# Kernel optimization log

Hardware: AMD Instinct MI355X
Metric: run time of the kernel (lower is better)

Reference implementation:

```python
import jax, jax.numpy as jnp
import numpy as np

B, L, D, H = 2, 2048, 1024, 16
HD = D // H

def setup_inputs() -> dict:
    key = jax.random.key(0)
    ks = jax.random.split(key, 9)
    s = 1.0 / np.sqrt(D)
    return {
        "x": jax.random.normal(ks[0], (B, L, D), jnp.float32),
        "Wq": jax.random.normal(ks[1], (D, D), jnp.float32) * s,
        "bq": jax.random.normal(ks[2], (D,), jnp.float32) * 0.02,
        "Wk": jax.random.normal(ks[3], (D, D), jnp.float32) * s,
        "bk": jax.random.normal(ks[4], (D,), jnp.float32) * 0.02,
        "Wv": jax.random.normal(ks[5], (D, D), jnp.float32) * s,
        "bv": jax.random.normal(ks[6], (D,), jnp.float32) * 0.02,
        "Wo": jax.random.normal(ks[7], (D, D), jnp.float32) * s,
        "bo": jax.random.normal(ks[8], (D,), jnp.float32) * 0.02,
    }

def reference(x, Wq, bq, Wk, bk, Wv, bv, Wo, bo):
    b, l, d = x.shape
    # projections -> [B, H, L, HD]
    def split_heads(t):
        return t.reshape(b, l, H, HD).transpose(0, 2, 1, 3)
    Q = split_heads(x @ Wq + bq)
    K = split_heads(x @ Wk + bk)
    V = split_heads(x @ Wv + bv)
    scores = jnp.einsum('bhqd,bhkd->bhqk', Q, K)  # [B,H,L,L]
    causal = jnp.tril(jnp.ones((l, l), bool))
    scores = jnp.where(causal, scores, -jnp.inf)
    attn = jax.nn.softmax(scores / np.sqrt(HD), axis=-1)
    ctx = jnp.einsum('bhqk,bhkd->bhqd', attn, V)
    ctx = ctx.transpose(0, 2, 1, 3).reshape(b, l, d)
    return ctx @ Wo + bo
```

## Files before the change

### kernel.cpp

```cpp
#include <hip/hip_runtime.h>
#include <stdint.h>

typedef unsigned short u16;
typedef __attribute__((ext_vector_type(8))) __bf16 bf16x8;
typedef __attribute__((ext_vector_type(4))) float f32x4;

#define BM 128
#define BN 128
#define BK 32

__device__ __forceinline__ u16 f2bf(float f) {
  union { float f; uint32_t u; } c; c.f = f;
  uint32_t u = c.u + 0x7fffu + ((c.u >> 16) & 1u);
  return (u16)(u >> 16);
}
__device__ __forceinline__ uint32_t cvtpk(float a, float b) {
  uint32_t r;
  asm("v_cvt_pk_bf16_f32 %0, %1, %2" : "=v"(r) : "v"(a), "v"(b));
  return r;
}

__device__ __forceinline__ void async16(const u16* g, u16* l) {
  __builtin_amdgcn_global_load_lds(
      (const __attribute__((address_space(1))) void*)g,
      (__attribute__((address_space(3))) void*)l, 16, 0, 0);
}

__device__ __forceinline__ f32x4 mfma16(bf16x8 a, bf16x8 b, f32x4 c) {
  return __builtin_amdgcn_mfma_f32_16x16x32_bf16(a, b, c, 0, 0, 0);
}


__global__ __launch_bounds__(256) void x_cvt_kernel(const float* __restrict__ x,
                                                    u16* __restrict__ xb) {
  int i = (blockIdx.x * 256 + threadIdx.x) * 4;
  float4 v = *(const float4*)(x + i);
  uint2 t; t.x = cvtpk(v.x, v.y); t.y = cvtpk(v.z, v.w);
  *(uint2*)(xb + i) = t;
}

__global__ __launch_bounds__(256) void wt_cvt_kernel(const float* __restrict__ Wq,
                                                     const float* __restrict__ Wk,
                                                     const float* __restrict__ Wv,
                                                     const float* __restrict__ Wo,
                                                     u16* __restrict__ out) {
  __shared__ __align__(16) u16 t[64][72];
  int z = blockIdx.z;
  const float* W = (z == 0) ? Wq : (z == 1) ? Wk : (z == 2) ? Wv : Wo;
  u16* o = out + (size_t)z * (1u << 20);
  int n0 = blockIdx.x * 64, k0 = blockIdx.y * 64;
  int tid = threadIdx.x;
  int c4 = (tid & 15) * 4, r0 = tid >> 4;
#pragma unroll
  for (int i = 0; i < 4; i++) {
    int r = r0 + i * 16;
    float4 v = *(const float4*)(W + (size_t)(k0 + r) * 1024 + n0 + c4);
    t[c4 + 0][r] = f2bf(v.x);
    t[c4 + 1][r] = f2bf(v.y);
    t[c4 + 2][r] = f2bf(v.z);
    t[c4 + 3][r] = f2bf(v.w);
  }
  __syncthreads();
  int n = tid >> 2, kc = (tid & 3) * 16;
  uint4 a = *(const uint4*)&t[n][kc];
  uint4 b = *(const uint4*)&t[n][kc + 8];
  *(uint4*)(o + (size_t)(n0 + n) * 1024 + k0 + kc) = a;
  *(uint4*)(o + (size_t)(n0 + n) * 1024 + k0 + kc + 8) = b;
}


__device__ __forceinline__ void gemm_core(const u16* __restrict__ A,
                                          const u16* __restrict__ Bt,
                                          u16* As, u16* Bs, f32x4 (&acc)[4][4]) {
  const int tid = threadIdx.x, wave = tid >> 6, lane = tid & 63;
  const int low = lane & 15, hi = lane >> 4;
  const int wm = wave >> 1, wn = wave & 1;
  const int m0 = blockIdx.y * BM, n0 = blockIdx.x * BN;
  const f32x4 fzero = {0.f, 0.f, 0.f, 0.f};
#pragma unroll
  for (int i = 0; i < 4; i++)
#pragma unroll
    for (int j = 0; j < 4; j++) acc[i][j] = fzero;

  const u16* ap = As + (wm * 64 + low) * BK + hi * 8;
  const u16* bp = Bs + (wn * 64 + low) * BK + hi * 8;

  const int e0 = wave * 128 + lane;
  const int e1 = e0 + 64;
  const u16* ga0 = A + (size_t)(m0 + (e0 >> 2)) * 1024 + (e0 & 3) * 8;
  const u16* ga1 = A + (size_t)(m0 + (e1 >> 2)) * 1024 + (e1 & 3) * 8;
  const u16* gb0 = Bt + (size_t)(n0 + (e0 >> 2)) * 1024 + (e0 & 3) * 8;
  const u16* gb1 = Bt + (size_t)(n0 + (e1 >> 2)) * 1024 + (e1 & 3) * 8;
  u16* la0 = As + (wave * 2 + 0) * 512;
  u16* la1 = As + (wave * 2 + 1) * 512;
  u16* lb0 = Bs + (wave * 2 + 0) * 512;
  u16* lb1 = Bs + (wave * 2 + 1) * 512;

  for (int kt = 0; kt < 1024; kt += BK) {
    __syncthreads();
    async16(ga0 + kt, la0);
    async16(ga1 + kt, la1);
    async16(gb0 + kt, lb0);
    async16(gb1 + kt, lb1);
    __syncthreads();
    bf16x8 af[4], bfv[4];
#pragma unroll
    for (int i = 0; i < 4; i++) af[i] = *(const bf16x8*)(ap + i * 16 * BK);
#pragma unroll
    for (int j = 0; j < 4; j++) bfv[j] = *(const bf16x8*)(bp + j * 16 * BK);
#pragma unroll
    for (int i = 0; i < 4; i++)
#pragma unroll
      for (int j = 0; j < 4; j++) acc[i][j] = mfma16(af[i], bfv[j], acc[i][j]);
  }
}

__global__ __launch_bounds__(256) void gemm_qkv_kernel(
    const u16* __restrict__ xb, const u16* __restrict__ wT,
    const float* __restrict__ bq, const float* __restrict__ bk,
    const float* __restrict__ bv,
    u16* __restrict__ qs, u16* __restrict__ ks, u16* __restrict__ vts) {
  __shared__ __align__(16) u16 As[BM * BK];
  __shared__ __align__(16) u16 Bs[BN * BK];
  const int z = blockIdx.z;
  const u16* Bt = wT + (size_t)z * (1u << 20);
  f32x4 acc[4][4];
  gemm_core(xb, Bt, As, Bs, acc);

  const float* bias = (z == 0) ? bq : (z == 1) ? bk : bv;
  u16* out = (z == 0) ? qs : (z == 1) ? ks : vts;
  const float scale = (z == 0) ? 0.180336880f : 1.0f;
  const int tid = threadIdx.x, wave = tid >> 6, lane = tid & 63;
  const int low = lane & 15, hi = lane >> 4;
  const int wm = wave >> 1, wn = wave & 1;
  const int m0 = blockIdx.y * BM, n0 = blockIdx.x * BN;
#pragma unroll
  for (int i = 0; i < 4; i++)
#pragma unroll
    for (int j = 0; j < 4; j++) {
      int gn = n0 + wn * 64 + j * 16 + low;
      float bval = bias[gn];
      int h = gn >> 6, hd = gn & 63;
#pragma unroll
      for (int r = 0; r < 4; r++) {
        int gm = m0 + wm * 64 + i * 16 + hi * 4 + r;
        int b = gm >> 11, l = gm & 2047;
        float v = (acc[i][j][r] + bval) * scale;
        size_t addr;
        if (z == 2) addr = ((size_t)((b * 16 + h) * 64 + hd)) * 2048 + l;
        else        addr = ((size_t)((b * 16 + h) * 2048 + l)) * 64 + hd;
        out[addr] = f2bf(v);
      }
    }
}

__global__ __launch_bounds__(256) void gemm_out_kernel(
    const u16* __restrict__ ctx, const u16* __restrict__ woT,
    const float* __restrict__ bo, float* __restrict__ out) {
  __shared__ __align__(16) u16 As[BM * BK];
  __shared__ __align__(16) u16 Bs[BN * BK];
  f32x4 acc[4][4];
  gemm_core(ctx, woT, As, Bs, acc);
  const int tid = threadIdx.x, wave = tid >> 6, lane = tid & 63;
  const int low = lane & 15, hi = lane >> 4;
  const int wm = wave >> 1, wn = wave & 1;
  const int m0 = blockIdx.y * BM, n0 = blockIdx.x * BN;
#pragma unroll
  for (int i = 0; i < 4; i++)
#pragma unroll
    for (int j = 0; j < 4; j++) {
      int gn = n0 + wn * 64 + j * 16 + low;
      float bval = bo[gn];
#pragma unroll
      for (int r = 0; r < 4; r++) {
        int gm = m0 + wm * 64 + i * 16 + hi * 4 + r;
        out[(size_t)gm * 1024 + gn] = acc[i][j][r] + bval;
      }
    }
}

#define PSTR 72

__global__ __launch_bounds__(256) void flash_kernel(
    const u16* __restrict__ Qs, const u16* __restrict__ Ks,
    const u16* __restrict__ Vts, u16* __restrict__ ctx) {
  __shared__ __align__(16) u16 Kls[3][64 * 64];
  __shared__ __align__(16) u16 Vls[3][64 * 64];
  __shared__ __align__(16) u16 Pls[8][16 * PSTR];

  const int bid = blockIdx.x;
  const int qt = 15 - (bid >> 5);
  const int bh = bid & 31;
  const int qb = qt * 128;
  const int nkv = 2 * qt + 2;

  const int tid = threadIdx.x, wave = tid >> 6, lane = tid & 63;
  const int low = lane & 15, hi = lane >> 4;
  const int x7 = low & 7;

  const u16* Qb = Qs + (size_t)bh * (2048 * 64);
  const u16* Kb = Ks + (size_t)bh * (2048 * 64);
  const u16* Vb = Vts + (size_t)bh * (64 * 2048);
  const f32x4 fzero = {0.f, 0.f, 0.f, 0.f};

  bf16x8 qf[2][2];
#pragma unroll
  for (int sub = 0; sub < 2; sub++)
#pragma unroll
    for (int dh = 0; dh < 2; dh++)
      qf[sub][dh] = *(const bf16x8*)(Qb + (size_t)(qb + wave * 32 + sub * 16 + low) * 64 + dh * 32 + hi * 8);

  f32x4 o[2][4];
  float m_[2], l_[2];
#pragma unroll
  for (int sub = 0; sub < 2; sub++) {
    m_[sub] = -1e30f; l_[sub] = 0.f;
#pragma unroll
    for (int nt = 0; nt < 4; nt++) o[sub][nt] = fzero;
  }

  const int srow0 = (lane >> 3);
  const int scc = lane & 7;

#define STAGE(buf, KT0)                                                        \
  {                                                                            \
    _Pragma("unroll") for (int i = 0; i < 2; i++) {                            \
      int row = (wave * 2 + i) * 8 + srow0;                                    \
      async16(Kb + (size_t)((KT0) + row) * 64 + ((scc ^ (row & 7)) * 8),       \
              &Kls[buf][(wave * 2 + i) * 512]);                                \
      async16(Vb + (size_t)row * 2048 + (KT0) + ((scc ^ (row & 7)) * 8),       \
              &Vls[buf][(wave * 2 + i) * 512]);                                \
    }                                                                          \
  }

  STAGE(0, 0)
  STAGE(1, 64)

  u16* pls0 = &Pls[wave * 2 + 0][0];
  u16* pls1 = &Pls[wave * 2 + 1][0];
  const int qmax = qb + wave * 32 + 31;

  int c0 = 0, c1 = 1, c2 = 2;
  for (int t = 0; t < nkv; t++) {
    const int kt0 = t * 64;
    if (t + 1 < nkv) { asm volatile("s_waitcnt vmcnt(4)" ::: "memory"); }
    else             { asm volatile("s_waitcnt vmcnt(0)" ::: "memory"); }
    __builtin_amdgcn_s_barrier();
    if (t + 2 < nkv) STAGE(c2, kt0 + 128)

    if (kt0 <= qmax) {
      const u16* Kc = &Kls[c0][0];
      const u16* Vc = &Vls[c0][0];

      f32x4 s[2][4];
      __builtin_amdgcn_s_setprio(1);
#pragma unroll
      for (int nt = 0; nt < 4; nt++) {
        const u16* kb = Kc + (nt * 16 + low) * 64;
        bf16x8 kf0 = *(const bf16x8*)(kb + ((hi ^ x7) * 8));
        bf16x8 kf1 = *(const bf16x8*)(kb + (((4 + hi) ^ x7) * 8));
        s[0][nt] = mfma16(kf0, qf[0][0], fzero);
        s[0][nt] = mfma16(kf1, qf[0][1], s[0][nt]);
        s[1][nt] = mfma16(kf0, qf[1][0], fzero);
        s[1][nt] = mfma16(kf1, qf[1][1], s[1][nt]);
      }
      __builtin_amdgcn_s_setprio(0);

      bf16x8 vf[4][2];
#pragma unroll
      for (int ntd = 0; ntd < 4; ntd++) {
        const u16* vb = Vc + (ntd * 16 + low) * 64;
        vf[ntd][0] = *(const bf16x8*)(vb + ((hi ^ x7) * 8));
        vf[ntd][1] = *(const bf16x8*)(vb + (((4 + hi) ^ x7) * 8));
      }

#pragma unroll
      for (int sub = 0; sub < 2; sub++) {
        const int qsb = qb + wave * 32 + sub * 16;
        if (kt0 + 63 > qsb) {
          const int qrow = qsb + low;
#pragma unroll
          for (int nt = 0; nt < 4; nt++)
#pragma unroll
            for (int r = 0; r < 4; r++) {
              int kg = kt0 + nt * 16 + hi * 4 + r;
              if (kg > qrow) s[sub][nt][r] = -1e30f;
            }
        }
      }

      float pm[2];
#pragma unroll
      for (int sub = 0; sub < 2; sub++) {
        float p = -1e30f;
#pragma unroll
        for (int nt = 0; nt < 4; nt++)
#pragma unroll
          for (int r = 0; r < 4; r++) p = fmaxf(p, s[sub][nt][r]);
        p = fmaxf(p, __shfl_xor(p, 16));
        p = fmaxf(p, __shfl_xor(p, 32));
        pm[sub] = p;
      }
      if (__any((pm[0] > m_[0] + 8.f) || (pm[1] > m_[1] + 8.f))) {
#pragma unroll
        for (int sub = 0; sub < 2; sub++) {
          float mn = fmaxf(m_[sub], pm[sub]);
          float corr = __builtin_amdgcn_exp2f(m_[sub] - mn);
          m_[sub] = mn;
          l_[sub] *= corr;
#pragma unroll
          for (int nt = 0; nt < 4; nt++) {
            o[sub][nt][0] *= corr; o[sub][nt][1] *= corr;
            o[sub][nt][2] *= corr; o[sub][nt][3] *= corr;
          }
        }
      }

#pragma unroll
      for (int sub = 0; sub < 2; sub++) {
        float rs = 0.f;
        u16* pls = sub ? pls1 : pls0;
#pragma unroll
        for (int nt = 0; nt < 4; nt++) {
          float p0 = __builtin_amdgcn_exp2f(s[sub][nt][0] - m_[sub]);
          float p1 = __builtin_amdgcn_exp2f(s[sub][nt][1] - m_[sub]);
          float p2 = __builtin_amdgcn_exp2f(s[sub][nt][2] - m_[sub]);
          float p3 = __builtin_amdgcn_exp2f(s[sub][nt][3] - m_[sub]);
          rs += (p0 + p1) + (p2 + p3);
          uint2 w; w.x = cvtpk(p0, p1); w.y = cvtpk(p2, p3);
          *(uint2*)(pls + low * PSTR + nt * 16 + hi * 4) = w;
        }
        rs += __shfl_xor(rs, 16);
        rs += __shfl_xor(rs, 32);
        l_[sub] += rs;
      }
      asm volatile("s_waitcnt lgkmcnt(0)" ::: "memory");
      __builtin_amdgcn_sched_barrier(0);

      bf16x8 pb[2][2];
#pragma unroll
      for (int kc = 0; kc < 2; kc++) {
        pb[0][kc] = *(const bf16x8*)(pls0 + low * PSTR + kc * 32 + hi * 8);
        pb[1][kc] = *(const bf16x8*)(pls1 + low * PSTR + kc * 32 + hi * 8);
      }
      __builtin_amdgcn_s_setprio(1);
#pragma unroll
      for (int ntd = 0; ntd < 4; ntd++) {
        o[0][ntd] = mfma16(vf[ntd][0], pb[0][0], o[0][ntd]);
        o[0][ntd] = mfma16(vf[ntd][1], pb[0][1], o[0][ntd]);
        o[1][ntd] = mfma16(vf[ntd][0], pb[1][0], o[1][ntd]);
        o[1][ntd] = mfma16(vf[ntd][1], pb[1][1], o[1][ntd]);
      }
      __builtin_amdgcn_s_setprio(0);
    }

    int tmp = c0; c0 = c1; c1 = c2; c2 = tmp;
  }

  const int b = bh >> 4, h = bh & 15;
#pragma unroll
  for (int sub = 0; sub < 2; sub++) {
    float inv = 1.f / l_[sub];
    int qg = qb + wave * 32 + sub * 16 + low;
    size_t base = ((size_t)(b * 2048 + qg)) * 1024 + h * 64;
#pragma unroll
    for (int ntd = 0; ntd < 4; ntd++) {
      uint2 w;
      w.x = cvtpk(o[sub][ntd][0] * inv, o[sub][ntd][1] * inv);
      w.y = cvtpk(o[sub][ntd][2] * inv, o[sub][ntd][3] * inv);
      *(uint2*)(ctx + base + ntd * 16 + hi * 4) = w;
    }
  }
}


extern "C" void kernel_launch(void* const* d_in, const int* in_sizes, int n_in,
                              void* d_out, int out_size, void* d_ws, size_t ws_size,
                              hipStream_t stream) {
  const float* x  = (const float*)d_in[0];
  const float* Wq = (const float*)d_in[1];
  const float* bq = (const float*)d_in[2];
  const float* Wk = (const float*)d_in[3];
  const float* bk = (const float*)d_in[4];
  const float* Wv = (const float*)d_in[5];
  const float* bv = (const float*)d_in[6];
  const float* Wo = (const float*)d_in[7];
  const float* bo = (const float*)d_in[8];

  char* ws = (char*)d_ws;
  u16* xb  = (u16*)(ws);
  u16* wT  = (u16*)(ws + (8u << 20));
  u16* qs  = (u16*)(ws + (16u << 20));
  u16* ks  = (u16*)(ws + (24u << 20));
  u16* vts = (u16*)(ws + (32u << 20));
  u16* ctx = (u16*)(ws + (40u << 20));

  x_cvt_kernel<<<4096, 256, 0, stream>>>(x, xb);
  wt_cvt_kernel<<<dim3(16, 16, 4), 256, 0, stream>>>(Wq, Wk, Wv, Wo, wT);
  gemm_qkv_kernel<<<dim3(8, 32, 3), 256, 0, stream>>>(xb, wT, bq, bk, bv, qs, ks, vts);
  flash_kernel<<<512, 256, 0, stream>>>(qs, ks, vts, ctx);
  gemm_out_kernel<<<dim3(8, 32), 256, 0, stream>>>(ctx, wT + 3 * (1u << 20), bo, (float*)d_out);
}
```

Baseline: 133.3 us.

## Switch flash attention to 32x32x16 MFMA with register-resident P

Rewrites the flash attention inner loop to use 32x32x16 bf16 MFMA tiles, so each wave handles 32 query rows as one tile. The softmax output is packed straight into MFMA operand registers instead of going through an LDS round trip, which removes the P shared buffer and its waitcnt stall. It also changes the block-to-query-tile mapping for block ids of 256 and above. The risk is higher register pressure from the 16-wide accumulators and different LDS bank patterns on the V reads.

New measurement: 130.9 us. Within noise of the previous version (-1.8%).

```diff
diff --git a/kernel.cpp b/kernel.cpp
--- a/kernel.cpp
+++ b/kernel.cpp
@@ -4,6 +4,7 @@
 typedef unsigned short u16;
 typedef __attribute__((ext_vector_type(8))) __bf16 bf16x8;
 typedef __attribute__((ext_vector_type(4))) float f32x4;
+typedef __attribute__((ext_vector_type(16))) float f32x16;
 
 #define BM 128
 #define BN 128
@@ -28,6 +29,9 @@
 
 __device__ __forceinline__ f32x4 mfma16(bf16x8 a, bf16x8 b, f32x4 c) {
   return __builtin_amdgcn_mfma_f32_16x16x32_bf16(a, b, c, 0, 0, 0);
+}
+__device__ __forceinline__ f32x16 mfma32(bf16x8 a, bf16x8 b, f32x16 c) {
+  return __builtin_amdgcn_mfma_f32_32x32x16_bf16(a, b, c, 0, 0, 0);
 }
 
 
@@ -179,45 +183,36 @@
     }
 }
 
-#define PSTR 72
-
 __global__ __launch_bounds__(256) void flash_kernel(
     const u16* __restrict__ Qs, const u16* __restrict__ Ks,
     const u16* __restrict__ Vts, u16* __restrict__ ctx) {
   __shared__ __align__(16) u16 Kls[3][64 * 64];
   __shared__ __align__(16) u16 Vls[3][64 * 64];
-  __shared__ __align__(16) u16 Pls[8][16 * PSTR];
 
   const int bid = blockIdx.x;
-  const int qt = 15 - (bid >> 5);
+  const int qt = (bid < 256) ? (15 - (bid >> 5)) : ((bid - 256) >> 5);
   const int bh = bid & 31;
   const int qb = qt * 128;
   const int nkv = 2 * qt + 2;
 
   const int tid = threadIdx.x, wave = tid >> 6, lane = tid & 63;
-  const int low = lane & 15, hi = lane >> 4;
-  const int x7 = low & 7;
+  const int q32 = lane & 31, hi2 = lane >> 5;
+  const int x7 = q32 & 7;
 
   const u16* Qb = Qs + (size_t)bh * (2048 * 64);
   const u16* Kb = Ks + (size_t)bh * (2048 * 64);
   const u16* Vb = Vts + (size_t)bh * (64 * 2048);
-  const f32x4 fzero = {0.f, 0.f, 0.f, 0.f};
-
-  bf16x8 qf[2][2];
-#pragma unroll
-  for (int sub = 0; sub < 2; sub++)
-#pragma unroll
-    for (int dh = 0; dh < 2; dh++)
-      qf[sub][dh] = *(const bf16x8*)(Qb + (size_t)(qb + wave * 32 + sub * 16 + low) * 64 + dh * 32 + hi * 8);
-
-  f32x4 o[2][4];
-  float m_[2], l_[2];
-#pragma unroll
-  for (int sub = 0; sub < 2; sub++) {
-    m_[sub] = -1e30f; l_[sub] = 0.f;
-#pragma unroll
-    for (int nt = 0; nt < 4; nt++) o[sub][nt] = fzero;
-  }
+
+  const int qrow = qb + wave * 32 + q32;
+  bf16x8 qf[4];
+#pragma unroll
+  for (int ds = 0; ds < 4; ds++)
+    qf[ds] = *(const bf16x8*)(Qb + (size_t)qrow * 64 + ds * 16 + hi2 * 8);
+
+  f32x16 o0, o1;
+#pragma unroll
+  for (int r = 0; r < 16; r++) { o0[r] = 0.f; o1[r] = 0.f; }
+  float m_ = -1e30f, l_ = 0.f;
 
   const int srow0 = (lane >> 3);
   const int scc = lane & 7;
@@ -236,8 +231,6 @@
   STAGE(0, 0)
   STAGE(1, 64)
 
-  u16* pls0 = &Pls[wave * 2 + 0][0];
-  u16* pls1 = &Pls[wave * 2 + 1][0];
   const int qmax = qb + wave * 32 + 31;
 
   int c0 = 0, c1 = 1, c2 = 2;
@@ -252,104 +245,89 @@
       const u16* Kc = &Kls[c0][0];
       const u16* Vc = &Vls[c0][0];
 
-      f32x4 s[2][4];
+      f32x16 s0, s1;
+#pragma unroll
+      for (int r = 0; r < 16; r++) { s0[r] = 0.f; s1[r] = 0.f; }
       __builtin_amdgcn_s_setprio(1);
 #pragma unroll
-      for (int nt = 0; nt < 4; nt++) {
-        const u16* kb = Kc + (nt * 16 + low) * 64;
-        bf16x8 kf0 = *(const bf16x8*)(kb + ((hi ^ x7) * 8));
-        bf16x8 kf1 = *(const bf16x8*)(kb + (((4 + hi) ^ x7) * 8));
-        s[0][nt] = mfma16(kf0, qf[0][0], fzero);
-        s[0][nt] = mfma16(kf1, qf[0][1], s[0][nt]);
-        s[1][nt] = mfma16(kf0, qf[1][0], fzero);
-        s[1][nt] = mfma16(kf1, qf[1][1], s[1][nt]);
+      for (int ds = 0; ds < 4; ds++) {
+        int cc = ds * 2 + hi2;
+        bf16x8 kf0 = *(const bf16x8*)(Kc + q32 * 64 + ((cc ^ x7) * 8));
+        bf16x8 kf1 = *(const bf16x8*)(Kc + (32 + q32) * 64 + ((cc ^ x7) * 8));
+        s0 = mfma32(kf0, qf[ds], s0);
+        s1 = mfma32(kf1, qf[ds], s1);
       }
       __builtin_amdgcn_s_setprio(0);
 
-      bf16x8 vf[4][2];
-#pragma unroll
-      for (int ntd = 0; ntd < 4; ntd++) {
-        const u16* vb = Vc + (ntd * 16 + low) * 64;
-        vf[ntd][0] = *(const bf16x8*)(vb + ((hi ^ x7) * 8));
-        vf[ntd][1] = *(const bf16x8*)(vb + (((4 + hi) ^ x7) * 8));
-      }
-
-#pragma unroll
-      for (int sub = 0; sub < 2; sub++) {
-        const int qsb = qb + wave * 32 + sub * 16;
-        if (kt0 + 63 > qsb) {
-          const int qrow = qsb + low;
-#pragma unroll
-          for (int nt = 0; nt < 4; nt++)
-#pragma unroll
-            for (int r = 0; r < 4; r++) {
-              int kg = kt0 + nt * 16 + hi * 4 + r;
-              if (kg > qrow) s[sub][nt][r] = -1e30f;
-            }
+      bf16x8 vf0[4], vf1[4];
+#pragma unroll
+      for (int ks = 0; ks < 4; ks++) {
+        int ca = (2 * ks) ^ x7, cb = (2 * ks + 1) ^ x7;
+        union { uint2 u[2]; bf16x8 v; } a, b;
+        a.u[0] = *(const uint2*)(Vc + q32 * 64 + ca * 8 + 4 * hi2);
+        a.u[1] = *(const uint2*)(Vc + q32 * 64 + cb * 8 + 4 * hi2);
+        b.u[0] = *(const uint2*)(Vc + (32 + q32) * 64 + ca * 8 + 4 * hi2);
+        b.u[1] = *(const uint2*)(Vc + (32 + q32) * 64 + cb * 8 + 4 * hi2);
+        vf0[ks] = a.v; vf1[ks] = b.v;
+      }
+
+      if (kt0 + 63 > qb + wave * 32) {
+#pragma unroll
+        for (int r = 0; r < 16; r++) {
+          int kl = (r & 3) + 8 * (r >> 2) + 4 * hi2;
+          if (kt0 + kl > qrow) s0[r] = -1e30f;
+          if (kt0 + 32 + kl > qrow) s1[r] = -1e30f;
         }
       }
 
-      float pm[2];
-#pragma unroll
-      for (int sub = 0; sub < 2; sub++) {
-        float p = -1e30f;
-#pragma unroll
-        for (int nt = 0; nt < 4; nt++)
-#pragma unroll
-          for (int r = 0; r < 4; r++) p = fmaxf(p, s[sub][nt][r]);
-        p = fmaxf(p, __shfl_xor(p, 16));
-        p = fmaxf(p, __shfl_xor(p, 32));
-        pm[sub] = p;
-      }
-      if (__any((pm[0] > m_[0] + 8.f) || (pm[1] > m_[1] + 8.f))) {
-#pragma unroll
-        for (int sub = 0; sub < 2; sub++) {
-          float mn = fmaxf(m_[sub], pm[sub]);
-          float corr = __builtin_amdgcn_exp2f(m_[sub] - mn);
-          m_[sub] = mn;
-          l_[sub] *= corr;
-#pragma unroll
-          for (int nt = 0; nt < 4; nt++) {
-            o[sub][nt][0] *= corr; o[sub][nt][1] *= corr;
-            o[sub][nt][2] *= corr; o[sub][nt][3] *= corr;
-          }
+      float pm = -1e30f;
+#pragma unroll
+      for (int r = 0; r < 16; r++) pm = fmaxf(pm, fmaxf(s0[r], s1[r]));
+      pm = fmaxf(pm, __shfl_xor(pm, 32));
+      if (__any(pm > m_ + 8.f)) {
+        float mn = fmaxf(m_, pm);
+        float corr = __builtin_amdgcn_exp2f(m_ - mn);
+        m_ = mn;
+        l_ *= corr;
+#pragma unroll
+        for (int r = 0; r < 16; r++) { o0[r] *= corr; o1[r] *= corr; }
+      }
+
+      float rs = 0.f;
+#pragma unroll
+      for (int r = 0; r < 16; r++) {
+        s0[r] = __builtin_amdgcn_exp2f(s0[r] - m_);
+        s1[r] = __builtin_amdgcn_exp2f(s1[r] - m_);
+        rs += s0[r] + s1[r];
+      }
+      rs += __shfl_xor(rs, 32);
+      l_ += rs;
+
+      bf16x8 pb[4];
+#pragma unroll
+      for (int ks = 0; ks < 4; ks++) {
+        union { uint32_t u[4]; bf16x8 v; } pu;
+        if (ks < 2) {
+          int rb = 8 * ks;
+          pu.u[0] = cvtpk(s0[rb + 0], s0[rb + 1]);
+          pu.u[1] = cvtpk(s0[rb + 2], s0[rb + 3]);
+          pu.u[2] = cvtpk(s0[rb + 4], s0[rb + 5]);
+          pu.u[3] = cvtpk(s0[rb + 6], s0[rb + 7]);
+        } else {
+          int rb = 8 * (ks - 2);
+          pu.u[0] = cvtpk(s1[rb + 0], s1[rb + 1]);
+          pu.u[1] = cvtpk(s1[rb + 2], s1[rb + 3]);
+          pu.u[2] = cvtpk(s1[rb + 4], s1[rb + 5]);
+          pu.u[3] = cvtpk(s1[rb + 6], s1[rb + 7]);
         }
-      }
-
-#pragma unroll
-      for (int sub = 0; sub < 2; sub++) {
-        float rs = 0.f;
-        u16* pls = sub ? pls1 : pls0;
-#pragma unroll
-        for (int nt = 0; nt < 4; nt++) {
-          float p0 = __builtin_amdgcn_exp2f(s[sub][nt][0] - m_[sub]);
-          float p1 = __builtin_amdgcn_exp2f(s[sub][nt][1] - m_[sub]);
-          float p2 = __builtin_amdgcn_exp2f(s[sub][nt][2] - m_[sub]);
-          float p3 = __builtin_amdgcn_exp2f(s[sub][nt][3] - m_[sub]);
-          rs += (p0 + p1) + (p2 + p3);
-          uint2 w; w.x = cvtpk(p0, p1); w.y = cvtpk(p2, p3);
-          *(uint2*)(pls + low * PSTR + nt * 16 + hi * 4) = w;
-        }
-        rs += __shfl_xor(rs, 16);
-        rs += __shfl_xor(rs, 32);
-        l_[sub] += rs;
-      }
-      asm volatile("s_waitcnt lgkmcnt(0)" ::: "memory");
-      __builtin_amdgcn_sched_barrier(0);
-
-      bf16x8 pb[2][2];
-#pragma unroll
-      for (int kc = 0; kc < 2; kc++) {
-        pb[0][kc] = *(const bf16x8*)(pls0 + low * PSTR + kc * 32 + hi * 8);
-        pb[1][kc] = *(const bf16x8*)(pls1 + low * PSTR + kc * 32 + hi * 8);
-      }
+        pb[ks] = pu.v;
+      }
+
       __builtin_amdgcn_s_setprio(1);
 #pragma unroll
-      for (int ntd = 0; ntd < 4; ntd++) {
-        o[0][ntd] = mfma16(vf[ntd][0], pb[0][0], o[0][ntd]);
-        o[0][ntd] = mfma16(vf[ntd][1], pb[0][1], o[0][ntd]);
-        o[1][ntd] = mfma16(vf[ntd][0], pb[1][0], o[1][ntd]);
-        o[1][ntd] = mfma16(vf[ntd][1], pb[1][1], o[1][ntd]);
+      for (int ks = 0; ks < 4; ks++) {
+        o0 = mfma32(vf0[ks], pb[ks], o0);
+        o1 = mfma32(vf1[ks], pb[ks], o1);
       }
       __builtin_amdgcn_s_setprio(0);
     }
@@ -358,18 +336,17 @@
   }
 
   const int b = bh >> 4, h = bh & 15;
-#pragma unroll
-  for (int sub = 0; sub < 2; sub++) {
-    float inv = 1.f / l_[sub];
-    int qg = qb + wave * 32 + sub * 16 + low;
-    size_t base = ((size_t)(b * 2048 + qg)) * 1024 + h * 64;
-#pragma unroll
-    for (int ntd = 0; ntd < 4; ntd++) {
-      uint2 w;
-      w.x = cvtpk(o[sub][ntd][0] * inv, o[sub][ntd][1] * inv);
-      w.y = cvtpk(o[sub][ntd][2] * inv, o[sub][ntd][3] * inv);
-      *(uint2*)(ctx + base + ntd * 16 + hi * 4) = w;
-    }
+  float inv = 1.f / l_;
+  size_t base = ((size_t)(b * 2048 + qrow)) * 1024 + h * 64;
+#pragma unroll
+  for (int m = 0; m < 4; m++) {
+    uint2 w0, w1;
+    w0.x = cvtpk(o0[4 * m + 0] * inv, o0[4 * m + 1] * inv);
+    w0.y = cvtpk(o0[4 * m + 2] * inv, o0[4 * m + 3] * inv);
+    *(uint2*)(ctx + base + 8 * m + 4 * hi2) = w0;
+    w1.x = cvtpk(o1[4 * m + 0] * inv, o1[4 * m + 1] * inv);
+    w1.y = cvtpk(o1[4 * m + 2] * inv, o1[4 * m + 3] * inv);
+    *(uint2*)(ctx + base + 32 + 8 * m + 4 * hi2) = w1;
   }
 }
 
```
